# Kernel optimization log

Measured on AMD Instinct MI355X. Metric: run time of the kernel, lower is better.

The kernel has to match this reference:

```python
import jax, jax.numpy as jnp
import numpy as np

B, S, DIM = 2, 2048, 2048
H, KVH, HD = 16, 4, 128
G = H // KVH  # GQA groups = 4
THETA = 10000.0


def setup_inputs() -> dict:
    key = jax.random.key(0)
    k0, k1, k2, k3, k4 = jax.random.split(key, 5)
    x = jax.random.normal(k0, (B, S, DIM), jnp.float32)
    # RoPE table: [max_seq_len, head_dim//2, 2] holding (cos, sin)
    inv_freq = 1.0 / (THETA ** (jnp.arange(0, HD, 2, dtype=jnp.float32) / HD))
    angles = jnp.outer(jnp.arange(S, dtype=jnp.float32), inv_freq)  # [S, HD//2]
    freqs_cis = jnp.stack([jnp.cos(angles), jnp.sin(angles)], axis=-1)
    sc = 0.02
    wq = jax.random.normal(k1, (H * HD, DIM), jnp.float32) * sc
    wk = jax.random.normal(k2, (KVH * HD, DIM), jnp.float32) * sc
    wv = jax.random.normal(k3, (KVH * HD, DIM), jnp.float32) * sc
    wo = jax.random.normal(k4, (DIM, H * HD), jnp.float32) * sc
    return {"x": x, "freqs_cis": freqs_cis, "wq": wq, "wk": wk, "wv": wv, "wo": wo}


def apply_rope(x, freqs_cis):
    # x: [B, S, h, HD]; freqs_cis: [max_S, HD//2, 2]
    s = x.shape[1]
    xr = x.astype(jnp.float32).reshape(*x.shape[:-1], -1, 2)  # [B,S,h,HD//2,2]
    cos = freqs_cis[:s, :, 0][None, :, None, :]  # [1,S,1,HD//2]
    sin = freqs_cis[:s, :, 1][None, :, None, :]
    x0, x1 = xr[..., 0], xr[..., 1]
    out = jnp.stack([x0 * cos - x1 * sin, x0 * sin + x1 * cos], axis=-1)
    return out.reshape(x.shape).astype(x.dtype)


def reference(x, freqs_cis, wq, wk, wv, wo):
    b, s, d = x.shape
    q = (x @ wq.T).reshape(b, s, H, HD)
    k = (x @ wk.T).reshape(b, s, KVH, HD)
    v = (x @ wv.T).reshape(b, s, KVH, HD)
    q = apply_rope(q, freqs_cis)
    k = apply_rope(k, freqs_cis)
    # GQA expand: repeat_interleave along head dim
    k = jnp.repeat(k, G, axis=2)  # [b,s,H,HD]
    v = jnp.repeat(v, G, axis=2)
    q = jnp.swapaxes(q, 1, 2)  # [b,H,s,HD]
    k = jnp.swapaxes(k, 1, 2)
    v = jnp.swapaxes(v, 1, 2)
    scale = 1.0 / jnp.sqrt(jnp.asarray(HD, dtype=q.dtype))
    scores = jnp.einsum('bhqd,bhkd->bhqk', q, k) * scale  # [b,H,s,s]
    causal = jnp.tril(jnp.ones((s, s), dtype=bool))
    scores = jnp.where(causal[None, None], scores, jnp.finfo(scores.dtype).min)
    probs = jax.nn.softmax(scores, axis=-1)
    attn = jnp.einsum('bhqk,bhkd->bhqd', probs, v)  # [b,H,s,HD]
    attn = jnp.swapaxes(attn, 1, 2).reshape(b, s, H * HD)
    return attn @ wo.T
```

## Files before the change

kernel.cpp:

```cpp
#include <hip/hip_runtime.h>
#include <stdint.h>

#define B_ 2
#define S_ 2048
#define DIM_ 2048
#define H_ 16
#define KVH_ 4
#define HD_ 128

typedef short short8 __attribute__((ext_vector_type(8)));
typedef float f4 __attribute__((ext_vector_type(4)));
typedef unsigned short u16;

__device__ __forceinline__ float bf2f(u16 u) {
    union { unsigned int i; float f; } c; c.i = ((unsigned int)u) << 16; return c.f;
}
__device__ __forceinline__ u16 f2bf(float f) {
    union { float f; unsigned int i; } c; c.f = f;
    return (u16)((c.i + 0x7fffu + ((c.i >> 16) & 1u)) >> 16);
}

#define GLDS16(gp, lp) \
    __builtin_amdgcn_global_load_lds((const __attribute__((address_space(1))) unsigned int*)(gp), \
                                     (__attribute__((address_space(3))) unsigned int*)(lp), 16, 0, 0)

__global__ void cast4_kernel(const float* __restrict__ in, u16* __restrict__ out, int n4) {
    int i = blockIdx.x * blockDim.x + threadIdx.x;
    if (i < n4) {
        float4 v = ((const float4*)in)[i];
        ushort4 o;
        o.x = f2bf(v.x); o.y = f2bf(v.y); o.z = f2bf(v.z); o.w = f2bf(v.w);
        ((ushort4*)out)[i] = o;
    }
}

template<bool OUT_BF16>
__global__ __launch_bounds__(256) void gemm_bt(const u16* __restrict__ A,
                                               const u16* __restrict__ W,
                                               void* __restrict__ Cout,
                                               int M, int N, int K) {
    __shared__ u16 As[128 * 32];
    __shared__ u16 Bs[128 * 32];
    int t = threadIdx.x, lane = t & 63, w = t >> 6;
    int quad = lane >> 4, l16 = lane & 15;
    int wm = w & 1, wn = w >> 1;
    size_t m0 = (size_t)blockIdx.y * 128, n0 = (size_t)blockIdx.x * 128;

    int c0 = w * 2;
    int ar = c0 * 16 + (lane >> 2);
    int ac = (lane & 3) * 8;
    const u16* Abase = A + (m0 + ar) * (size_t)K + ac;
    const u16* Bbase = W + (n0 + ar) * (size_t)K + ac;
    u16* Adst = As + c0 * 512;
    u16* Bdst = Bs + c0 * 512;

    f4 acc[4][4];
    #pragma unroll
    for (int i = 0; i < 4; i++)
        #pragma unroll
        for (int j = 0; j < 4; j++) acc[i][j] = (f4){0.f, 0.f, 0.f, 0.f};

    int nk = K >> 5;
    for (int kt = 0; kt < nk; kt++) {
        const u16* ga = Abase + kt * 32;
        const u16* gb = Bbase + kt * 32;
        GLDS16(ga, Adst);
        GLDS16(ga + 16 * (size_t)K, Adst + 512);
        GLDS16(gb, Bdst);
        GLDS16(gb + 16 * (size_t)K, Bdst + 512);
        __syncthreads();
        short8 a[4], b[4];
        #pragma unroll
        for (int i = 0; i < 4; i++) a[i] = *(const short8*)&As[(wm * 64 + i * 16 + l16) * 32 + quad * 8];
        #pragma unroll
        for (int j = 0; j < 4; j++) b[j] = *(const short8*)&Bs[(wn * 64 + j * 16 + l16) * 32 + quad * 8];
        #pragma unroll
        for (int i = 0; i < 4; i++)
            #pragma unroll
            for (int j = 0; j < 4; j++)
                acc[i][j] = __builtin_amdgcn_mfma_f32_16x16x32_bf16(a[i], b[j], acc[i][j], 0, 0, 0);
        __syncthreads();
    }
    #pragma unroll
    for (int i = 0; i < 4; i++) {
        size_t row = m0 + wm * 64 + i * 16 + quad * 4;
        #pragma unroll
        for (int j = 0; j < 4; j++) {
            size_t col = n0 + wn * 64 + j * 16 + l16;
            #pragma unroll
            for (int r = 0; r < 4; r++) {
                if (OUT_BF16) ((u16*)Cout)[(row + r) * N + col] = f2bf(acc[i][j][r]);
                else          ((float*)Cout)[(row + r) * N + col] = acc[i][j][r];
            }
        }
    }
}

__global__ void rope_kernel(u16* __restrict__ QKV, const float* __restrict__ freqs) {
    int pc = blockIdx.x * 256 + threadIdx.x;
    int row = blockIdx.y;
    int s = row & (S_ - 1);
    int hd2 = pc & 63;
    float2 cs = ((const float2*)freqs)[s * 64 + hd2];
    ushort2* pp = (ushort2*)(QKV + (size_t)row * 3072);
    ushort2 v = pp[pc];
    float x0 = bf2f(v.x), x1 = bf2f(v.y);
    ushort2 ov;
    ov.x = f2bf(x0 * cs.x - x1 * cs.y);
    ov.y = f2bf(x0 * cs.y + x1 * cs.x);
    pp[pc] = ov;
}

__global__ __launch_bounds__(256) void pack_k(const u16* __restrict__ QKV, u16* __restrict__ Kp) {
    int gid = blockIdx.x * 256 + threadIdx.x;
    int lane = gid & 63;
    int fid = (gid >> 6) & 15;
    int kt = (gid >> 10) & 31;
    int bk = gid >> 15;
    int b = bk >> 2, kvh = bk & 3;
    int n = fid >> 2, c = fid & 3;
    int l16 = lane & 15, quad = lane >> 4;
    int s = kt * 64 + n * 16 + l16;
    const u16* src = QKV + (size_t)(b * 2048 + s) * 3072 + 2048 + kvh * 128 + c * 32 + quad * 8;
    *(short8*)&Kp[(size_t)gid * 8] = *(const short8*)src;
}

__global__ __launch_bounds__(256) void pack_v(const u16* __restrict__ QKV, u16* __restrict__ Vp) {
    int gid = blockIdx.x * 256 + threadIdx.x;
    int lane = gid & 63;
    int fid = (gid >> 6) & 15;
    int kt = (gid >> 10) & 31;
    int bk = gid >> 15;
    int b = bk >> 2, kvh = bk & 3;
    int nt = fid >> 1, kc = fid & 1;
    int l16 = lane & 15, quad = lane >> 4;
    int hd = nt * 16 + l16;
    int s0 = kt * 64 + kc * 32 + quad * 8;
    const u16* src = QKV + (size_t)(b * 2048 + s0) * 3072 + 2560 + kvh * 128 + hd;
    short8 v;
    #pragma unroll
    for (int j = 0; j < 8; j++) v[j] = (short)src[(size_t)j * 3072];
    *(short8*)&Vp[(size_t)gid * 8] = v;
}

__global__ __launch_bounds__(256, 4) void attn_kernel(const u16* __restrict__ QKV,
                                                      const u16* __restrict__ Kp,
                                                      const u16* __restrict__ Vp,
                                                      u16* __restrict__ Ob) {
    __shared__ u16 Ks[16 * 512];
    __shared__ u16 Vs[16 * 512];
    __shared__ u16 Ps[4 * 2048];
    int bid = blockIdx.x;
    int bk = bid & 7;
    int qt = 127 - (bid >> 3);
    int b = bk >> 2, kvh = bk & 3;
    int t = threadIdx.x, lane = t & 63, w = t >> 6, quad = lane >> 4, l16 = lane & 15;
    int l7 = l16 & 7, hi = l16 >> 3;
    int h = kvh * 4 + w;
    const float kscale = 0.08838834764831845f * 1.4426950408889634f;

    short8 qf[4];
    {
        const u16* qp = QKV + ((size_t)(b * S_ + qt * 16 + l16)) * 3072 + h * HD_ + quad * 8;
        #pragma unroll
        for (int c = 0; c < 4; c++) qf[c] = *(const short8*)(qp + c * 32);
    }
    short8 ones;
    #pragma unroll
    for (int j = 0; j < 8; j++) ones[j] = (short)0x3F80;

    float m_i[4];
    f4 ls = (f4){0.f, 0.f, 0.f, 0.f};
    f4 o[8];
    #pragma unroll
    for (int r = 0; r < 4; r++) m_i[r] = -1e30f;
    #pragma unroll
    for (int n = 0; n < 8; n++) o[n] = (f4){0.f, 0.f, 0.f, 0.f};

    const u16* Kpb = Kp + (size_t)bk * 32 * 8192;
    const u16* Vpb = Vp + (size_t)bk * 32 * 8192;
    u16* P = Ps + w * 2048;
    int nkt = (qt >> 2) + 1;

    for (int kt = 0; kt < nkt; kt++) {
        {
            const u16* ks = Kpb + (size_t)kt * 8192 + (w * 4) * 512 + lane * 8;
            const u16* vs = Vpb + (size_t)kt * 8192 + (w * 4) * 512 + lane * 8;
            #pragma unroll
            for (int i = 0; i < 4; i++) {
                GLDS16(ks + i * 512, &Ks[(w * 4 + i) * 512]);
                GLDS16(vs + i * 512, &Vs[(w * 4 + i) * 512]);
            }
        }
        __syncthreads();

        f4 sc[4];
        #pragma unroll
        for (int n = 0; n < 4; n++) sc[n] = (f4){0.f, 0.f, 0.f, 0.f};
        #pragma unroll
        for (int n = 0; n < 4; n++) {
            #pragma unroll
            for (int c = 0; c < 4; c++) {
                short8 kf = *(const short8*)&Ks[(n * 4 + c) * 512 + lane * 8];
                sc[n] = __builtin_amdgcn_mfma_f32_16x16x32_bf16(qf[c], kf, sc[n], 0, 0, 0);
            }
        }
        if (kt == nkt - 1) {
            int qrow0 = qt * 16 + quad * 4;
            #pragma unroll
            for (int n = 0; n < 4; n++) {
                int colg = kt * 64 + n * 16 + l16;
                #pragma unroll
                for (int r = 0; r < 4; r++)
                    sc[n][r] = (colg <= qrow0 + r) ? sc[n][r] : -1e30f;
            }
        }
        float mnew[4];
        bool chg = false;
        #pragma unroll
        for (int r = 0; r < 4; r++) {
            float mx = fmaxf(fmaxf(sc[0][r], sc[1][r]), fmaxf(sc[2][r], sc[3][r]));
            #pragma unroll
            for (int off = 1; off < 16; off <<= 1) mx = fmaxf(mx, __shfl_xor(mx, off, 64));
            mnew[r] = fmaxf(m_i[r], mx);
            chg |= (mnew[r] > m_i[r]);
        }
        if (__ballot(chg)) {
            #pragma unroll
            for (int r = 0; r < 4; r++) {
                float al = exp2f((m_i[r] - mnew[r]) * kscale);
                m_i[r] = mnew[r];
                ls[r] *= al;
                #pragma unroll
                for (int nt = 0; nt < 8; nt++) o[nt][r] *= al;
            }
        }
        float mk[4];
        #pragma unroll
        for (int r = 0; r < 4; r++) mk[r] = m_i[r] * kscale;
        #pragma unroll
        for (int n = 0; n < 4; n++) {
            #pragma unroll
            for (int r = 0; r < 4; r++) {
                float p = exp2f(__builtin_fmaf(sc[n][r], kscale, -mk[r]));
                union { float f; unsigned int u; } cv; cv.f = p;
                int row = quad * 4 + r;
                int sw = (n * 2 + hi) ^ (row & 7);
                P[row * 64 + sw * 8 + l7] = (u16)(cv.u >> 16);
            }
        }
        __asm__ volatile("s_waitcnt lgkmcnt(0)" ::: "memory");

        #pragma unroll
        for (int kc = 0; kc < 2; kc++) {
            short8 af = *(const short8*)&P[l16 * 64 + (((kc * 4 + quad) ^ l7) << 3)];
            ls = __builtin_amdgcn_mfma_f32_16x16x32_bf16(af, ones, ls, 0, 0, 0);
            #pragma unroll
            for (int nt = 0; nt < 8; nt++) {
                short8 vf = *(const short8*)&Vs[(nt * 2 + kc) * 512 + lane * 8];
                o[nt] = __builtin_amdgcn_mfma_f32_16x16x32_bf16(af, vf, o[nt], 0, 0, 0);
            }
        }
        __syncthreads();
    }
    float rl[4];
    #pragma unroll
    for (int r = 0; r < 4; r++) rl[r] = 1.0f / ls[r];
    #pragma unroll
    for (int nt = 0; nt < 8; nt++)
        #pragma unroll
        for (int r = 0; r < 4; r++) {
            size_t row = (size_t)b * S_ + qt * 16 + quad * 4 + r;
            Ob[row * 2048 + h * HD_ + nt * 16 + l16] = f2bf(o[nt][r] * rl[r]);
        }
}

extern "C" void kernel_launch(void* const* d_in, const int* in_sizes, int n_in,
                              void* d_out, int out_size, void* d_ws, size_t ws_size,
                              hipStream_t stream) {
    const float* x     = (const float*)d_in[0];
    const float* freqs = (const float*)d_in[1];
    const float* wq    = (const float*)d_in[2];
    const float* wk    = (const float*)d_in[3];
    const float* wv    = (const float*)d_in[4];
    const float* wo    = (const float*)d_in[5];
    float* out = (float*)d_out;

    char* p = (char*)d_ws;
    u16* xb    = (u16*)p; p += (size_t)4096 * 2048 * 2;
    u16* wqkvb = (u16*)p; p += (size_t)3072 * 2048 * 2;
    u16* wob   = (u16*)p; p += (size_t)2048 * 2048 * 2;
    u16* QKVb  = (u16*)p; p += (size_t)4096 * 3072 * 2;
    u16* Kpb   = (u16*)p; p += (size_t)8 * 32 * 8192 * 2;
    u16* Vpb   = (u16*)p; p += (size_t)8 * 32 * 8192 * 2;
    u16* attnb = xb;

    cast4_kernel<<<8192, 256, 0, stream>>>(x, xb, 2097152);
    cast4_kernel<<<4096, 256, 0, stream>>>(wq, wqkvb, 1048576);
    cast4_kernel<<<1024, 256, 0, stream>>>(wk, wqkvb + (size_t)2048 * 2048, 262144);
    cast4_kernel<<<1024, 256, 0, stream>>>(wv, wqkvb + (size_t)2560 * 2048, 262144);
    cast4_kernel<<<4096, 256, 0, stream>>>(wo, wob, 1048576);

    gemm_bt<true><<<dim3(24, 32), 256, 0, stream>>>(xb, wqkvb, QKVb, 4096, 3072, 2048);

    rope_kernel<<<dim3(5, 4096), 256, 0, stream>>>(QKVb, freqs);

    pack_k<<<1024, 256, 0, stream>>>(QKVb, Kpb);
    pack_v<<<1024, 256, 0, stream>>>(QKVb, Vpb);

    attn_kernel<<<1024, 256, 0, stream>>>(QKVb, Kpb, Vpb, attnb);

    gemm_bt<false><<<dim3(16, 32), 256, 0, stream>>>(attnb, wob, out, 4096, 2048, 2048);
}
```

Baseline: 344.6 us.

## Pair short and long causal query tiles per block, fuse K RoPE into packing

Each attention block now handles two query tiles, qt and 127-qt, sharing K/V tile loads so every block does the same amount of causal work, and the grid is halved. The Q RoPE kernel folds the softmax scale into Q, and K RoPE moves into the K packing kernel, which removes a pass over K. V packing now transposes through LDS with coalesced reads instead of strided global loads. The running max becomes one value per wave instead of per row, which saves shuffles but risks precision loss when rows in a tile differ widely; the extra registers for the second tile also lower occupancy to 3 waves.

```diff
diff --git a/kernel.cpp b/kernel.cpp
--- a/kernel.cpp
+++ b/kernel.cpp
@@ -11,6 +11,8 @@
 typedef short short8 __attribute__((ext_vector_type(8)));
 typedef float f4 __attribute__((ext_vector_type(4)));
 typedef unsigned short u16;
+
+#define KSCALE (0.08838834764831845f * 1.4426950408889634f)
 
 __device__ __forceinline__ float bf2f(u16 u) {
     union { unsigned int i; float f; } c; c.i = ((unsigned int)u) << 16; return c.f;
@@ -96,7 +98,7 @@
     }
 }
 
-__global__ void rope_kernel(u16* __restrict__ QKV, const float* __restrict__ freqs) {
+__global__ void rope_q(u16* __restrict__ QKV, const float* __restrict__ freqs) {
     int pc = blockIdx.x * 256 + threadIdx.x;
     int row = blockIdx.y;
     int s = row & (S_ - 1);
@@ -106,12 +108,14 @@
     ushort2 v = pp[pc];
     float x0 = bf2f(v.x), x1 = bf2f(v.y);
     ushort2 ov;
-    ov.x = f2bf(x0 * cs.x - x1 * cs.y);
-    ov.y = f2bf(x0 * cs.y + x1 * cs.x);
+    ov.x = f2bf((x0 * cs.x - x1 * cs.y) * KSCALE);
+    ov.y = f2bf((x0 * cs.y + x1 * cs.x) * KSCALE);
     pp[pc] = ov;
 }
 
-__global__ __launch_bounds__(256) void pack_k(const u16* __restrict__ QKV, u16* __restrict__ Kp) {
+__global__ __launch_bounds__(256) void pack_k(const u16* __restrict__ QKV,
+                                              const float* __restrict__ freqs,
+                                              u16* __restrict__ Kp) {
     int gid = blockIdx.x * 256 + threadIdx.x;
     int lane = gid & 63;
     int fid = (gid >> 6) & 15;
@@ -122,67 +126,88 @@
     int l16 = lane & 15, quad = lane >> 4;
     int s = kt * 64 + n * 16 + l16;
     const u16* src = QKV + (size_t)(b * 2048 + s) * 3072 + 2048 + kvh * 128 + c * 32 + quad * 8;
-    *(short8*)&Kp[(size_t)gid * 8] = *(const short8*)src;
+    short8 v = *(const short8*)src;
+    short8 o;
+    #pragma unroll
+    for (int jp = 0; jp < 4; jp++) {
+        int hd2 = c * 16 + quad * 4 + jp;
+        float2 cw = ((const float2*)freqs)[s * 64 + hd2];
+        float x0 = bf2f((u16)v[2 * jp]), x1 = bf2f((u16)v[2 * jp + 1]);
+        o[2 * jp]     = (short)f2bf(x0 * cw.x - x1 * cw.y);
+        o[2 * jp + 1] = (short)f2bf(x0 * cw.y + x1 * cw.x);
+    }
+    *(short8*)&Kp[(size_t)gid * 8] = o;
 }
 
 __global__ __launch_bounds__(256) void pack_v(const u16* __restrict__ QKV, u16* __restrict__ Vp) {
-    int gid = blockIdx.x * 256 + threadIdx.x;
-    int lane = gid & 63;
-    int fid = (gid >> 6) & 15;
-    int kt = (gid >> 10) & 31;
-    int bk = gid >> 15;
+    __shared__ u16 L[64 * 136];
+    int bid = blockIdx.x;
+    int bk = bid & 7, kt = bid >> 3;
     int b = bk >> 2, kvh = bk & 3;
-    int nt = fid >> 1, kc = fid & 1;
-    int l16 = lane & 15, quad = lane >> 4;
-    int hd = nt * 16 + l16;
-    int s0 = kt * 64 + kc * 32 + quad * 8;
-    const u16* src = QKV + (size_t)(b * 2048 + s0) * 3072 + 2560 + kvh * 128 + hd;
-    short8 v;
-    #pragma unroll
-    for (int j = 0; j < 8; j++) v[j] = (short)src[(size_t)j * 3072];
-    *(short8*)&Vp[(size_t)gid * 8] = v;
-}
-
-__global__ __launch_bounds__(256, 4) void attn_kernel(const u16* __restrict__ QKV,
+    int t = threadIdx.x;
+    const u16* src = QKV + (size_t)(b * 2048 + kt * 64) * 3072 + 2560 + kvh * 128;
+    #pragma unroll
+    for (int it = 0; it < 4; it++) {
+        int idx = t + it * 256;
+        int r = idx >> 4, c = idx & 15;
+        *(short8*)&L[r * 136 + c * 8] = *(const short8*)(src + (size_t)r * 3072 + c * 8);
+    }
+    __syncthreads();
+    u16* dst = Vp + ((size_t)bk * 32 + kt) * 8192;
+    #pragma unroll
+    for (int it = 0; it < 4; it++) {
+        int idx = t + it * 256;
+        int fid = idx >> 6, lane = idx & 63;
+        int nt = fid >> 1, kc = fid & 1;
+        int l16 = lane & 15, quad = lane >> 4;
+        int hd = nt * 16 + l16;
+        int s0 = kc * 32 + quad * 8;
+        short8 v;
+        #pragma unroll
+        for (int j = 0; j < 8; j++) v[j] = (short)L[(s0 + j) * 136 + hd];
+        *(short8*)&dst[(size_t)idx * 8] = v;
+    }
+}
+
+__global__ __launch_bounds__(256, 3) void attn_kernel(const u16* __restrict__ QKV,
                                                       const u16* __restrict__ Kp,
                                                       const u16* __restrict__ Vp,
                                                       u16* __restrict__ Ob) {
     __shared__ u16 Ks[16 * 512];
     __shared__ u16 Vs[16 * 512];
-    __shared__ u16 Ps[4 * 2048];
+    __shared__ u16 Ps[8192];
     int bid = blockIdx.x;
-    int bk = bid & 7;
-    int qt = 127 - (bid >> 3);
+    int bk = bid & 7, pr = bid >> 3;
     int b = bk >> 2, kvh = bk & 3;
+    int qtS = pr, qtL = 127 - pr;
+    int nktS = (qtS >> 2) + 1, nktL = (qtL >> 2) + 1;
     int t = threadIdx.x, lane = t & 63, w = t >> 6, quad = lane >> 4, l16 = lane & 15;
     int l7 = l16 & 7, hi = l16 >> 3;
     int h = kvh * 4 + w;
-    const float kscale = 0.08838834764831845f * 1.4426950408889634f;
-
-    short8 qf[4];
+
+    short8 qfL[4], qfS[4];
     {
-        const u16* qp = QKV + ((size_t)(b * S_ + qt * 16 + l16)) * 3072 + h * HD_ + quad * 8;
-        #pragma unroll
-        for (int c = 0; c < 4; c++) qf[c] = *(const short8*)(qp + c * 32);
+        const u16* qpL = QKV + ((size_t)(b * S_ + qtL * 16 + l16)) * 3072 + h * HD_ + quad * 8;
+        const u16* qpS = QKV + ((size_t)(b * S_ + qtS * 16 + l16)) * 3072 + h * HD_ + quad * 8;
+        #pragma unroll
+        for (int c = 0; c < 4; c++) { qfL[c] = *(const short8*)(qpL + c * 32); qfS[c] = *(const short8*)(qpS + c * 32); }
     }
     short8 ones;
     #pragma unroll
     for (int j = 0; j < 8; j++) ones[j] = (short)0x3F80;
 
-    float m_i[4];
-    f4 ls = (f4){0.f, 0.f, 0.f, 0.f};
-    f4 o[8];
-    #pragma unroll
-    for (int r = 0; r < 4; r++) m_i[r] = -1e30f;
-    #pragma unroll
-    for (int n = 0; n < 8; n++) o[n] = (f4){0.f, 0.f, 0.f, 0.f};
+    float mL = -3e38f, mS = -3e38f;
+    f4 lsL = (f4){0.f,0.f,0.f,0.f}, lsS = (f4){0.f,0.f,0.f,0.f};
+    f4 oL[8], oS[8];
+    #pragma unroll
+    for (int n = 0; n < 8; n++) { oL[n] = (f4){0.f,0.f,0.f,0.f}; oS[n] = (f4){0.f,0.f,0.f,0.f}; }
 
     const u16* Kpb = Kp + (size_t)bk * 32 * 8192;
     const u16* Vpb = Vp + (size_t)bk * 32 * 8192;
-    u16* P = Ps + w * 2048;
-    int nkt = (qt >> 2) + 1;
-
-    for (int kt = 0; kt < nkt; kt++) {
+    u16* PL = Ps + w * 1024;
+    u16* PS = Ps + 4096 + w * 1024;
+
+    for (int kt = 0; kt < nktL; kt++) {
         {
             const u16* ks = Kpb + (size_t)kt * 8192 + (w * 4) * 512 + lane * 8;
             const u16* vs = Vpb + (size_t)kt * 8192 + (w * 4) * 512 + lane * 8;
@@ -193,85 +218,132 @@
             }
         }
         __syncthreads();
-
-        f4 sc[4];
-        #pragma unroll
-        for (int n = 0; n < 4; n++) sc[n] = (f4){0.f, 0.f, 0.f, 0.f};
+        bool doS = (kt < nktS);
+
+        f4 scL[4], scS[4];
+        #pragma unroll
+        for (int n = 0; n < 4; n++) { scL[n] = (f4){0.f,0.f,0.f,0.f}; scS[n] = (f4){0.f,0.f,0.f,0.f}; }
         #pragma unroll
         for (int n = 0; n < 4; n++) {
             #pragma unroll
             for (int c = 0; c < 4; c++) {
                 short8 kf = *(const short8*)&Ks[(n * 4 + c) * 512 + lane * 8];
-                sc[n] = __builtin_amdgcn_mfma_f32_16x16x32_bf16(qf[c], kf, sc[n], 0, 0, 0);
-            }
-        }
-        if (kt == nkt - 1) {
-            int qrow0 = qt * 16 + quad * 4;
+                scL[n] = __builtin_amdgcn_mfma_f32_16x16x32_bf16(qfL[c], kf, scL[n], 0, 0, 0);
+                if (doS) scS[n] = __builtin_amdgcn_mfma_f32_16x16x32_bf16(qfS[c], kf, scS[n], 0, 0, 0);
+            }
+        }
+
+        {
+            if (kt == nktL - 1) {
+                int qrow0 = qtL * 16 + quad * 4;
+                #pragma unroll
+                for (int n = 0; n < 4; n++) {
+                    int colg = kt * 64 + n * 16 + l16;
+                    #pragma unroll
+                    for (int r = 0; r < 4; r++)
+                        scL[n][r] = (colg <= qrow0 + r) ? scL[n][r] : -3e38f;
+                }
+            }
+            float gm = fmaxf(fmaxf(scL[0][0], scL[0][1]), fmaxf(scL[0][2], scL[0][3]));
+            #pragma unroll
+            for (int n = 1; n < 4; n++)
+                gm = fmaxf(gm, fmaxf(fmaxf(scL[n][0], scL[n][1]), fmaxf(scL[n][2], scL[n][3])));
+            #pragma unroll
+            for (int off = 1; off < 64; off <<= 1) gm = fmaxf(gm, __shfl_xor(gm, off, 64));
+            float mnew = fmaxf(mL, gm);
+            if (mnew > mL) {
+                float al = exp2f(mL - mnew);
+                mL = mnew;
+                #pragma unroll
+                for (int r = 0; r < 4; r++) lsL[r] *= al;
+                #pragma unroll
+                for (int nt = 0; nt < 8; nt++)
+                    #pragma unroll
+                    for (int r = 0; r < 4; r++) oL[nt][r] *= al;
+            }
             #pragma unroll
             for (int n = 0; n < 4; n++) {
-                int colg = kt * 64 + n * 16 + l16;
-                #pragma unroll
-                for (int r = 0; r < 4; r++)
-                    sc[n][r] = (colg <= qrow0 + r) ? sc[n][r] : -1e30f;
-            }
-        }
-        float mnew[4];
-        bool chg = false;
-        #pragma unroll
-        for (int r = 0; r < 4; r++) {
-            float mx = fmaxf(fmaxf(sc[0][r], sc[1][r]), fmaxf(sc[2][r], sc[3][r]));
-            #pragma unroll
-            for (int off = 1; off < 16; off <<= 1) mx = fmaxf(mx, __shfl_xor(mx, off, 64));
-            mnew[r] = fmaxf(m_i[r], mx);
-            chg |= (mnew[r] > m_i[r]);
-        }
-        if (__ballot(chg)) {
-            #pragma unroll
-            for (int r = 0; r < 4; r++) {
-                float al = exp2f((m_i[r] - mnew[r]) * kscale);
-                m_i[r] = mnew[r];
-                ls[r] *= al;
-                #pragma unroll
-                for (int nt = 0; nt < 8; nt++) o[nt][r] *= al;
-            }
-        }
-        float mk[4];
-        #pragma unroll
-        for (int r = 0; r < 4; r++) mk[r] = m_i[r] * kscale;
-        #pragma unroll
-        for (int n = 0; n < 4; n++) {
-            #pragma unroll
-            for (int r = 0; r < 4; r++) {
-                float p = exp2f(__builtin_fmaf(sc[n][r], kscale, -mk[r]));
-                union { float f; unsigned int u; } cv; cv.f = p;
-                int row = quad * 4 + r;
-                int sw = (n * 2 + hi) ^ (row & 7);
-                P[row * 64 + sw * 8 + l7] = (u16)(cv.u >> 16);
+                #pragma unroll
+                for (int r = 0; r < 4; r++) {
+                    float p = exp2f(scL[n][r] - mL);
+                    union { float f; unsigned int u; } cv; cv.f = p;
+                    int row = quad * 4 + r;
+                    int sw = (n * 2 + hi) ^ (row & 7);
+                    PL[row * 64 + sw * 8 + l7] = (u16)(cv.u >> 16);
+                }
+            }
+        }
+        if (doS) {
+            if (kt == nktS - 1) {
+                int qrow0 = qtS * 16 + quad * 4;
+                #pragma unroll
+                for (int n = 0; n < 4; n++) {
+                    int colg = kt * 64 + n * 16 + l16;
+                    #pragma unroll
+                    for (int r = 0; r < 4; r++)
+                        scS[n][r] = (colg <= qrow0 + r) ? scS[n][r] : -3e38f;
+                }
+            }
+            float gm = fmaxf(fmaxf(scS[0][0], scS[0][1]), fmaxf(scS[0][2], scS[0][3]));
+            #pragma unroll
+            for (int n = 1; n < 4; n++)
+                gm = fmaxf(gm, fmaxf(fmaxf(scS[n][0], scS[n][1]), fmaxf(scS[n][2], scS[n][3])));
+            #pragma unroll
+            for (int off = 1; off < 64; off <<= 1) gm = fmaxf(gm, __shfl_xor(gm, off, 64));
+            float mnew = fmaxf(mS, gm);
+            if (mnew > mS) {
+                float al = exp2f(mS - mnew);
+                mS = mnew;
+                #pragma unroll
+                for (int r = 0; r < 4; r++) lsS[r] *= al;
+                #pragma unroll
+                for (int nt = 0; nt < 8; nt++)
+                    #pragma unroll
+                    for (int r = 0; r < 4; r++) oS[nt][r] *= al;
+            }
+            #pragma unroll
+            for (int n = 0; n < 4; n++) {
+                #pragma unroll
+                for (int r = 0; r < 4; r++) {
+                    float p = exp2f(scS[n][r] - mS);
+                    union { float f; unsigned int u; } cv; cv.f = p;
+                    int row = quad * 4 + r;
+                    int sw = (n * 2 + hi) ^ (row & 7);
+                    PS[row * 64 + sw * 8 + l7] = (u16)(cv.u >> 16);
+                }
             }
         }
         __asm__ volatile("s_waitcnt lgkmcnt(0)" ::: "memory");
 
         #pragma unroll
         for (int kc = 0; kc < 2; kc++) {
-            short8 af = *(const short8*)&P[l16 * 64 + (((kc * 4 + quad) ^ l7) << 3)];
-            ls = __builtin_amdgcn_mfma_f32_16x16x32_bf16(af, ones, ls, 0, 0, 0);
+            short8 aL = *(const short8*)&PL[l16 * 64 + (((kc * 4 + quad) ^ l7) << 3)];
+            lsL = __builtin_amdgcn_mfma_f32_16x16x32_bf16(aL, ones, lsL, 0, 0, 0);
+            short8 aS;
+            if (doS) {
+                aS = *(const short8*)&PS[l16 * 64 + (((kc * 4 + quad) ^ l7) << 3)];
+                lsS = __builtin_amdgcn_mfma_f32_16x16x32_bf16(aS, ones, lsS, 0, 0, 0);
+            }
             #pragma unroll
             for (int nt = 0; nt < 8; nt++) {
                 short8 vf = *(const short8*)&Vs[(nt * 2 + kc) * 512 + lane * 8];
-                o[nt] = __builtin_amdgcn_mfma_f32_16x16x32_bf16(af, vf, o[nt], 0, 0, 0);
+                oL[nt] = __builtin_amdgcn_mfma_f32_16x16x32_bf16(aL, vf, oL[nt], 0, 0, 0);
+                if (doS) oS[nt] = __builtin_amdgcn_mfma_f32_16x16x32_bf16(aS, vf, oS[nt], 0, 0, 0);
             }
         }
         __syncthreads();
     }
-    float rl[4];
-    #pragma unroll
-    for (int r = 0; r < 4; r++) rl[r] = 1.0f / ls[r];
+    float rlL[4], rlS[4];
+    #pragma unroll
+    for (int r = 0; r < 4; r++) { rlL[r] = 1.0f / lsL[r]; rlS[r] = 1.0f / lsS[r]; }
     #pragma unroll
     for (int nt = 0; nt < 8; nt++)
         #pragma unroll
         for (int r = 0; r < 4; r++) {
-            size_t row = (size_t)b * S_ + qt * 16 + quad * 4 + r;
-            Ob[row * 2048 + h * HD_ + nt * 16 + l16] = f2bf(o[nt][r] * rl[r]);
+            size_t rowL = (size_t)b * S_ + qtL * 16 + quad * 4 + r;
+            size_t rowS = (size_t)b * S_ + qtS * 16 + quad * 4 + r;
+            Ob[rowL * 2048 + h * HD_ + nt * 16 + l16] = f2bf(oL[nt][r] * rlL[r]);
+            Ob[rowS * 2048 + h * HD_ + nt * 16 + l16] = f2bf(oS[nt][r] * rlS[r]);
         }
 }
 
@@ -303,12 +375,12 @@
 
     gemm_bt<true><<<dim3(24, 32), 256, 0, stream>>>(xb, wqkvb, QKVb, 4096, 3072, 2048);
 
-    rope_kernel<<<dim3(5, 4096), 256, 0, stream>>>(QKVb, freqs);
-
-    pack_k<<<1024, 256, 0, stream>>>(QKVb, Kpb);
-    pack_v<<<1024, 256, 0, stream>>>(QKVb, Vpb);
-
-    attn_kernel<<<1024, 256, 0, stream>>>(QKVb, Kpb, Vpb, attnb);
+    rope_q<<<dim3(4, 4096), 256, 0, stream>>>(QKVb, freqs);
+
+    pack_k<<<1024, 256, 0, stream>>>(QKVb, freqs, Kpb);
+    pack_v<<<256, 256, 0, stream>>>(QKVb, Vpb);
+
+    attn_kernel<<<512, 256, 0, stream>>>(QKVb, Kpb, Vpb, attnb);
 
     gemm_bt<false><<<dim3(16, 32), 256, 0, stream>>>(attnb, wob, out, 4096, 2048, 2048);
 }
```

Measured after the change: 414.3 us. 1.2x slower.

## Fold softmax scale into Q RoPE, fuse K RoPE into packing, LDS-transpose V

Applied to the files above, without the earlier changes.

Q RoPE now also multiplies by the softmax scale times log2(e), so the attention loop can drop its per-element FMA scaling. K RoPE is fused into pack_k, which avoids a separate read-modify-write pass over K. pack_v stages tiles through shared memory so global reads are coalesced instead of strided. Attention keeps one running max per wavefront rather than per row, which cuts shuffles and rescale work but risks underflow when rows in a tile differ widely in magnitude. Baking the scale into bf16 Q also shifts rounding slightly.

```diff
diff --git a/kernel.cpp b/kernel.cpp
--- a/kernel.cpp
+++ b/kernel.cpp
@@ -11,6 +11,8 @@
 typedef short short8 __attribute__((ext_vector_type(8)));
 typedef float f4 __attribute__((ext_vector_type(4)));
 typedef unsigned short u16;
+
+#define KSCALE (0.08838834764831845f * 1.4426950408889634f)
 
 __device__ __forceinline__ float bf2f(u16 u) {
     union { unsigned int i; float f; } c; c.i = ((unsigned int)u) << 16; return c.f;
@@ -96,7 +98,7 @@
     }
 }
 
-__global__ void rope_kernel(u16* __restrict__ QKV, const float* __restrict__ freqs) {
+__global__ void rope_q(u16* __restrict__ QKV, const float* __restrict__ freqs) {
     int pc = blockIdx.x * 256 + threadIdx.x;
     int row = blockIdx.y;
     int s = row & (S_ - 1);
@@ -106,12 +108,14 @@
     ushort2 v = pp[pc];
     float x0 = bf2f(v.x), x1 = bf2f(v.y);
     ushort2 ov;
-    ov.x = f2bf(x0 * cs.x - x1 * cs.y);
-    ov.y = f2bf(x0 * cs.y + x1 * cs.x);
+    ov.x = f2bf((x0 * cs.x - x1 * cs.y) * KSCALE);
+    ov.y = f2bf((x0 * cs.y + x1 * cs.x) * KSCALE);
     pp[pc] = ov;
 }
 
-__global__ __launch_bounds__(256) void pack_k(const u16* __restrict__ QKV, u16* __restrict__ Kp) {
+__global__ __launch_bounds__(256) void pack_k(const u16* __restrict__ QKV,
+                                              const float* __restrict__ freqs,
+                                              u16* __restrict__ Kp) {
     int gid = blockIdx.x * 256 + threadIdx.x;
     int lane = gid & 63;
     int fid = (gid >> 6) & 15;
@@ -122,25 +126,47 @@
     int l16 = lane & 15, quad = lane >> 4;
     int s = kt * 64 + n * 16 + l16;
     const u16* src = QKV + (size_t)(b * 2048 + s) * 3072 + 2048 + kvh * 128 + c * 32 + quad * 8;
-    *(short8*)&Kp[(size_t)gid * 8] = *(const short8*)src;
+    short8 v = *(const short8*)src;
+    short8 o;
+    #pragma unroll
+    for (int jp = 0; jp < 4; jp++) {
+        int hd2 = c * 16 + quad * 4 + jp;
+        float2 cw = ((const float2*)freqs)[s * 64 + hd2];
+        float x0 = bf2f((u16)v[2 * jp]), x1 = bf2f((u16)v[2 * jp + 1]);
+        o[2 * jp]     = (short)f2bf(x0 * cw.x - x1 * cw.y);
+        o[2 * jp + 1] = (short)f2bf(x0 * cw.y + x1 * cw.x);
+    }
+    *(short8*)&Kp[(size_t)gid * 8] = o;
 }
 
 __global__ __launch_bounds__(256) void pack_v(const u16* __restrict__ QKV, u16* __restrict__ Vp) {
-    int gid = blockIdx.x * 256 + threadIdx.x;
-    int lane = gid & 63;
-    int fid = (gid >> 6) & 15;
-    int kt = (gid >> 10) & 31;
-    int bk = gid >> 15;
+    __shared__ u16 L[64 * 136];
+    int bid = blockIdx.x;
+    int bk = bid & 7, kt = bid >> 3;
     int b = bk >> 2, kvh = bk & 3;
-    int nt = fid >> 1, kc = fid & 1;
-    int l16 = lane & 15, quad = lane >> 4;
-    int hd = nt * 16 + l16;
-    int s0 = kt * 64 + kc * 32 + quad * 8;
-    const u16* src = QKV + (size_t)(b * 2048 + s0) * 3072 + 2560 + kvh * 128 + hd;
-    short8 v;
-    #pragma unroll
-    for (int j = 0; j < 8; j++) v[j] = (short)src[(size_t)j * 3072];
-    *(short8*)&Vp[(size_t)gid * 8] = v;
+    int t = threadIdx.x;
+    const u16* src = QKV + (size_t)(b * 2048 + kt * 64) * 3072 + 2560 + kvh * 128;
+    #pragma unroll
+    for (int it = 0; it < 4; it++) {
+        int idx = t + it * 256;
+        int r = idx >> 4, c = idx & 15;
+        *(short8*)&L[r * 136 + c * 8] = *(const short8*)(src + (size_t)r * 3072 + c * 8);
+    }
+    __syncthreads();
+    u16* dst = Vp + ((size_t)bk * 32 + kt) * 8192;
+    #pragma unroll
+    for (int it = 0; it < 4; it++) {
+        int idx = t + it * 256;
+        int fid = idx >> 6, lane = idx & 63;
+        int nt = fid >> 1, kc = fid & 1;
+        int l16 = lane & 15, quad = lane >> 4;
+        int hd = nt * 16 + l16;
+        int s0 = kc * 32 + quad * 8;
+        short8 v;
+        #pragma unroll
+        for (int j = 0; j < 8; j++) v[j] = (short)L[(s0 + j) * 136 + hd];
+        *(short8*)&dst[(size_t)idx * 8] = v;
+    }
 }
 
 __global__ __launch_bounds__(256, 4) void attn_kernel(const u16* __restrict__ QKV,
@@ -149,7 +175,7 @@
                                                       u16* __restrict__ Ob) {
     __shared__ u16 Ks[16 * 512];
     __shared__ u16 Vs[16 * 512];
-    __shared__ u16 Ps[4 * 2048];
+    __shared__ u16 Ps[4 * 1024];
     int bid = blockIdx.x;
     int bk = bid & 7;
     int qt = 127 - (bid >> 3);
@@ -157,7 +183,6 @@
     int t = threadIdx.x, lane = t & 63, w = t >> 6, quad = lane >> 4, l16 = lane & 15;
     int l7 = l16 & 7, hi = l16 >> 3;
     int h = kvh * 4 + w;
-    const float kscale = 0.08838834764831845f * 1.4426950408889634f;
 
     short8 qf[4];
     {
@@ -169,17 +194,15 @@
     #pragma unroll
     for (int j = 0; j < 8; j++) ones[j] = (short)0x3F80;
 
-    float m_i[4];
+    float m_i = -3e38f;
     f4 ls = (f4){0.f, 0.f, 0.f, 0.f};
     f4 o[8];
     #pragma unroll
-    for (int r = 0; r < 4; r++) m_i[r] = -1e30f;
-    #pragma unroll
     for (int n = 0; n < 8; n++) o[n] = (f4){0.f, 0.f, 0.f, 0.f};
 
     const u16* Kpb = Kp + (size_t)bk * 32 * 8192;
     const u16* Vpb = Vp + (size_t)bk * 32 * 8192;
-    u16* P = Ps + w * 2048;
+    u16* P = Ps + w * 1024;
     int nkt = (qt >> 2) + 1;
 
     for (int kt = 0; kt < nkt; kt++) {
@@ -212,37 +235,31 @@
                 int colg = kt * 64 + n * 16 + l16;
                 #pragma unroll
                 for (int r = 0; r < 4; r++)
-                    sc[n][r] = (colg <= qrow0 + r) ? sc[n][r] : -1e30f;
-            }
-        }
-        float mnew[4];
-        bool chg = false;
-        #pragma unroll
-        for (int r = 0; r < 4; r++) {
-            float mx = fmaxf(fmaxf(sc[0][r], sc[1][r]), fmaxf(sc[2][r], sc[3][r]));
-            #pragma unroll
-            for (int off = 1; off < 16; off <<= 1) mx = fmaxf(mx, __shfl_xor(mx, off, 64));
-            mnew[r] = fmaxf(m_i[r], mx);
-            chg |= (mnew[r] > m_i[r]);
-        }
-        if (__ballot(chg)) {
+                    sc[n][r] = (colg <= qrow0 + r) ? sc[n][r] : -3e38f;
+            }
+        }
+        float gm = fmaxf(fmaxf(sc[0][0], sc[0][1]), fmaxf(sc[0][2], sc[0][3]));
+        #pragma unroll
+        for (int n = 1; n < 4; n++)
+            gm = fmaxf(gm, fmaxf(fmaxf(sc[n][0], sc[n][1]), fmaxf(sc[n][2], sc[n][3])));
+        #pragma unroll
+        for (int off = 1; off < 64; off <<= 1) gm = fmaxf(gm, __shfl_xor(gm, off, 64));
+        float mnew = fmaxf(m_i, gm);
+        if (mnew > m_i) {
+            float al = exp2f(m_i - mnew);
+            m_i = mnew;
+            #pragma unroll
+            for (int r = 0; r < 4; r++) ls[r] *= al;
+            #pragma unroll
+            for (int nt = 0; nt < 8; nt++)
+                #pragma unroll
+                for (int r = 0; r < 4; r++) o[nt][r] *= al;
+        }
+        #pragma unroll
+        for (int n = 0; n < 4; n++) {
             #pragma unroll
             for (int r = 0; r < 4; r++) {
-                float al = exp2f((m_i[r] - mnew[r]) * kscale);
-                m_i[r] = mnew[r];
-                ls[r] *= al;
-                #pragma unroll
-                for (int nt = 0; nt < 8; nt++) o[nt][r] *= al;
-            }
-        }
-        float mk[4];
-        #pragma unroll
-        for (int r = 0; r < 4; r++) mk[r] = m_i[r] * kscale;
-        #pragma unroll
-        for (int n = 0; n < 4; n++) {
-            #pragma unroll
-            for (int r = 0; r < 4; r++) {
-                float p = exp2f(__builtin_fmaf(sc[n][r], kscale, -mk[r]));
+                float p = exp2f(sc[n][r] - m_i);
                 union { float f; unsigned int u; } cv; cv.f = p;
                 int row = quad * 4 + r;
                 int sw = (n * 2 + hi) ^ (row & 7);
@@ -303,10 +320,10 @@
 
     gemm_bt<true><<<dim3(24, 32), 256, 0, stream>>>(xb, wqkvb, QKVb, 4096, 3072, 2048);
 
-    rope_kernel<<<dim3(5, 4096), 256, 0, stream>>>(QKVb, freqs);
-
-    pack_k<<<1024, 256, 0, stream>>>(QKVb, Kpb);
-    pack_v<<<1024, 256, 0, stream>>>(QKVb, Vpb);
+    rope_q<<<dim3(4, 4096), 256, 0, stream>>>(QKVb, freqs);
+
+    pack_k<<<1024, 256, 0, stream>>>(QKVb, freqs, Kpb);
+    pack_v<<<256, 256, 0, stream>>>(QKVb, Vpb);
 
     attn_kernel<<<1024, 256, 0, stream>>>(QKVb, Kpb, Vpb, attnb);
 
```

Result: no change. 345.6 us (+0.3%).
